# Kernel optimization log

Measured on AMD Instinct MI355X. Metric: run time of the kernel, lower is better.

## Reference

```python
import jax, jax.numpy as jnp
import numpy as np


def setup_inputs() -> dict:
    key = jax.random.key(0)
    ks = jax.random.split(key, 10)
    B, N, K, F, H, C, L = 2, 20000, 32, 128, 128, 40, 3
    return {
        "vertex_feat": jax.random.uniform(ks[0], (B, N, F), dtype=jnp.float32),
        "neighbors_idx": jax.random.randint(ks[1], (B, N, K), 0, N, dtype=jnp.int32),
        "valid_lens": jax.random.randint(ks[2], (B, N), 0, K + 1, dtype=jnp.int32),
        "W_embed": jax.random.normal(ks[3], (F, H), dtype=jnp.float32) * 0.05,
        "gcn_W": jax.random.normal(ks[4], (L, H, H), dtype=jnp.float32) * 0.05,
        "gcn_B": jax.random.normal(ks[5], (L, H, H), dtype=jnp.float32) * 0.05,
        "cls_W1": jax.random.normal(ks[6], (H, H), dtype=jnp.float32) * 0.05,
        "cls_b1": jnp.zeros((H,), dtype=jnp.float32),
        "cls_W2": jax.random.normal(ks[7], (H, C), dtype=jnp.float32) * 0.05,
        "cls_b2": jnp.zeros((C,), dtype=jnp.float32),
    }


def reference(vertex_feat, neighbors_idx, valid_lens, W_embed, gcn_W, gcn_B,
              cls_W1, cls_b1, cls_W2, cls_b2):
    # --- input embedding: Dense(no bias) / row-sum of raw features ---
    row_sum = jnp.sum(vertex_feat, axis=-1, keepdims=True)          # [B,N,1]
    h = jnp.einsum('bnf,fh->bnh', vertex_feat, W_embed) / row_sum   # [B,N,H]

    # valid_lens with zeros replaced by 1, as float divisor
    vl = jnp.where(valid_lens == 0, 1, valid_lens)
    vl = vl.astype(jnp.float32)[..., None]                          # [B,N,1]

    num_layers = gcn_W.shape[0]
    for l in range(num_layers):
        # gather-sum neighbor features (per-graph gather, batch_dims=1)
        neigh = jax.vmap(lambda feat, idx: feat[idx])(h, neighbors_idx)  # [B,N,K,H]
        neigh = jnp.sum(neigh, axis=2) / vl                              # [B,N,H]
        h = jax.nn.relu(jnp.einsum('bnh,hd->bnd', neigh, gcn_W[l])
                        + jnp.einsum('bnh,hd->bnd', h, gcn_B[l]))

    # --- classifier MLP (dropout inactive at inference) ---
    z = jax.nn.relu(jnp.einsum('bnh,hd->bnd', h, cls_W1) + cls_b1)
    logits = jnp.einsum('bnd,dc->bnc', z, cls_W2) + cls_b2
    return jax.nn.softmax(logits, axis=-1)
```

## Files before the change

kernel.cpp:

```cpp
#include <hip/hip_runtime.h>
#include <hip/hip_bf16.h>

typedef __hip_bfloat16 bf16;
typedef __attribute__((ext_vector_type(8))) short short8;
typedef __attribute__((ext_vector_type(4))) float f32x4;

#define NB    20000
#define BATCH 2
#define HDIM  128
#define KNBR  32
#define NCLS  40
#define NLAYER 3
#define BM    64
#define LBM   32
#define LDP   136
#define NTILES 625
#define LTPH   625
#define LGRID  1256

__device__ __forceinline__ short f2bf(float v) {
    return __builtin_bit_cast(short, __float2bfloat16(v));
}
__device__ __forceinline__ float blo(unsigned u) { return __builtin_bit_cast(float, u << 16); }
__device__ __forceinline__ float bhi(unsigned u) { return __builtin_bit_cast(float, u & 0xffff0000u); }

__global__ void pack_weights(const float* __restrict__ Wemb, const float* __restrict__ gW,
                             const float* __restrict__ gB, const float* __restrict__ W1,
                             const float* __restrict__ W2, short* __restrict__ pw) {
    const int idx = blockIdx.x * 256 + threadIdx.x;
    if (idx < 8 * 16384) {
        const int m = idx >> 14, e = idx & 16383;
        const float* src = (m == 0) ? Wemb
                         : (m <= 3) ? gW + (size_t)(m - 1) * 16384
                         : (m <= 6) ? gB + (size_t)(m - 4) * 16384
                         : W1;
        const int k = e >> 7, n = e & 127;
        pw[m * 16384 + (((k >> 3) * 128 + n) << 3) + (k & 7)] = f2bf(src[e]);
    } else {
        const int e = idx - 8 * 16384;
        if (e < 128 * NCLS) {
            const int k = e / NCLS, n = e - k * NCLS;
            pw[8 * 16384 + ((k >> 3) * NCLS + n) * 8 + (k & 7)] = f2bf(W2[e]);
        }
    }
}

__global__ __launch_bounds__(512, 4) void embed_gemm(const float* __restrict__ x,
                                                     const short* __restrict__ pwE,
                                                     bf16* __restrict__ h0) {
    __shared__ short sx[BM * LDP];
    const int t = threadIdx.x;
    const int row0 = blockIdx.x * BM;

    {
        const int r = t >> 3, fs = (t & 7) * 16;
        const float4* p = (const float4*)(x + (size_t)(row0 + r) * HDIM + fs);
        float4 v[4];
#pragma unroll
        for (int i = 0; i < 4; ++i) v[i] = p[i];
        const float* vf = (const float*)v;
        unsigned* dst = (unsigned*)(sx + r * LDP + fs);
#pragma unroll
        for (int i = 0; i < 8; ++i) {
            unsigned lo = (unsigned)(unsigned short)f2bf(vf[2 * i]);
            unsigned hi = (unsigned)(unsigned short)f2bf(vf[2 * i + 1]);
            dst[i] = lo | (hi << 16);
        }
    }
    __syncthreads();

    const int w = t >> 6, l = t & 63;
    const int m16 = l & 15, quad = l >> 4;
    const int col = w * 16 + m16;

    short8 ones;
#pragma unroll
    for (int j = 0; j < 8; ++j) ones[j] = (short)0x3F80;

    short8 wf[4];
#pragma unroll
    for (int q = 0; q < 4; ++q)
        wf[q] = *(const short8*)(pwE + (((q * 4 + quad) * 128 + col) << 3));

    f32x4 acc[4] = {}, rsum[4] = {};
#pragma unroll
    for (int q = 0; q < 4; ++q)
#pragma unroll
        for (int mt = 0; mt < 4; ++mt) {
            short8 a = *(const short8*)(sx + (mt * 16 + m16) * LDP + q * 32 + quad * 8);
            acc[mt]  = __builtin_amdgcn_mfma_f32_16x16x32_bf16(a, wf[q], acc[mt], 0, 0, 0);
            rsum[mt] = __builtin_amdgcn_mfma_f32_16x16x32_bf16(a, ones,  rsum[mt], 0, 0, 0);
        }

#pragma unroll
    for (int mt = 0; mt < 4; ++mt)
#pragma unroll
        for (int r = 0; r < 4; ++r) {
            const int rr = row0 + mt * 16 + quad * 4 + r;
            h0[(size_t)rr * HDIM + col] = __float2bfloat16(acc[mt][r] / rsum[mt][r]);
        }
}

__global__ __launch_bounds__(256, 4) void layer_gemm(const bf16* __restrict__ h_in,
                                                     const int* __restrict__ nidx,
                                                     const int* __restrict__ vlen,
                                                     const short* __restrict__ pwW,
                                                     const short* __restrict__ pwB,
                                                     bf16* __restrict__ h_out) {
    __shared__ int   sidx[LBM * KNBR];
    __shared__ short sng[LBM * LDP];
    __shared__ short sh[LBM * LDP];

    const int slot = blockIdx.x & 7;
    const int half = slot >> 2;
    const int idx  = (blockIdx.x >> 3) * 4 + (slot & 3);
    if (idx >= LTPH) return;
    const int tile = half * LTPH + idx;

    const int t = threadIdx.x;
    const int row0 = tile * LBM;

    ((int4*)sidx)[t] = ((const int4*)(nidx + (size_t)row0 * KNBR))[t];
    {
        const int r = t >> 3, fs = (t & 7) * 16;
        const uint4* p = (const uint4*)(h_in + (size_t)(row0 + r) * HDIM + fs);
        uint4 a = p[0], b = p[1];
        uint4* d = (uint4*)(sh + r * LDP + fs);
        d[0] = a; d[1] = b;
    }
    __syncthreads();

    {
        const int node = t >> 3;
        const int fs8 = (t & 7) * 8;
        const int g = row0 + node;
        const bf16* hb = h_in + (size_t)((g >= NB) ? NB : 0) * HDIM;
        const int* ip = sidx + node * KNBR;
        int vl = vlen[g]; if (vl == 0) vl = 1;
        const float inv = 1.0f / (float)vl;

#pragma unroll
        for (int fh = 0; fh < 2; ++fh) {
            const int fs = fh * 64 + fs8;
            float acc[8];
#pragma unroll
            for (int i = 0; i < 8; ++i) acc[i] = 0.0f;
#pragma unroll 4
            for (int k = 0; k < KNBR; ++k) {
                const uint4 u = *(const uint4*)(hb + (size_t)ip[k] * HDIM + fs);
                acc[0] += blo(u.x); acc[1] += bhi(u.x);
                acc[2] += blo(u.y); acc[3] += bhi(u.y);
                acc[4] += blo(u.z); acc[5] += bhi(u.z);
                acc[6] += blo(u.w); acc[7] += bhi(u.w);
            }
            unsigned* dst = (unsigned*)(sng + node * LDP + fs);
#pragma unroll
            for (int i = 0; i < 4; ++i) {
                unsigned lo = (unsigned)(unsigned short)f2bf(acc[2 * i] * inv);
                unsigned hi = (unsigned)(unsigned short)f2bf(acc[2 * i + 1] * inv);
                dst[i] = lo | (hi << 16);
            }
            __syncthreads();
        }
    }

    const int w = t >> 6, l = t & 63;
    const int m16 = l & 15, quad = l >> 4;
    const int ncol0 = w * 32;

    short8 wfW[2][4], wfB[2][4];
#pragma unroll
    for (int nt = 0; nt < 2; ++nt) {
        const int col = ncol0 + nt * 16 + m16;
#pragma unroll
        for (int q = 0; q < 4; ++q) {
            const int off = ((q * 4 + quad) * 128 + col) << 3;
            wfW[nt][q] = *(const short8*)(pwW + off);
            wfB[nt][q] = *(const short8*)(pwB + off);
        }
    }

    f32x4 acc[2][2] = {};
#pragma unroll
    for (int q = 0; q < 4; ++q)
#pragma unroll
        for (int mt = 0; mt < 2; ++mt) {
            short8 aN = *(const short8*)(sng + (mt * 16 + m16) * LDP + q * 32 + quad * 8);
            short8 aH = *(const short8*)(sh  + (mt * 16 + m16) * LDP + q * 32 + quad * 8);
#pragma unroll
            for (int nt = 0; nt < 2; ++nt) {
                acc[mt][nt] = __builtin_amdgcn_mfma_f32_16x16x32_bf16(aN, wfW[nt][q], acc[mt][nt], 0, 0, 0);
                acc[mt][nt] = __builtin_amdgcn_mfma_f32_16x16x32_bf16(aH, wfB[nt][q], acc[mt][nt], 0, 0, 0);
            }
        }

#pragma unroll
    for (int mt = 0; mt < 2; ++mt)
#pragma unroll
        for (int nt = 0; nt < 2; ++nt)
#pragma unroll
            for (int r = 0; r < 4; ++r) {
                const int rr = row0 + mt * 16 + quad * 4 + r;
                const int cc = ncol0 + nt * 16 + m16;
                h_out[(size_t)rr * HDIM + cc] = __float2bfloat16(fmaxf(acc[mt][nt][r], 0.0f));
            }
}

__global__ __launch_bounds__(512, 4) void cls_gemm(const bf16* __restrict__ h,
                                                   const short* __restrict__ pwW1,
                                                   const float* __restrict__ b1,
                                                   const short* __restrict__ pwW2,
                                                   const float* __restrict__ b2,
                                                   float* __restrict__ out) {
    __shared__ short sh[BM * LDP];
    __shared__ short sz[BM * LDP];
    __shared__ float lg[BM * 48];
    const int t = threadIdx.x;
    const int row0 = blockIdx.x * BM;

    {
        const int r = t >> 3, fs = (t & 7) * 16;
        const uint4* p = (const uint4*)(h + (size_t)(row0 + r) * HDIM + fs);
        uint4 a = p[0], b = p[1];
        uint4* d = (uint4*)(sh + r * LDP + fs);
        d[0] = a; d[1] = b;
    }
    __syncthreads();

    const int w = t >> 6, l = t & 63;
    const int m16 = l & 15, quad = l >> 4;
    const int col = w * 16 + m16;

    {
        short8 wf[4];
#pragma unroll
        for (int q = 0; q < 4; ++q)
            wf[q] = *(const short8*)(pwW1 + (((q * 4 + quad) * 128 + col) << 3));
        f32x4 acc[4] = {};
#pragma unroll
        for (int q = 0; q < 4; ++q)
#pragma unroll
            for (int mt = 0; mt < 4; ++mt) {
                short8 a = *(const short8*)(sh + (mt * 16 + m16) * LDP + q * 32 + quad * 8);
                acc[mt] = __builtin_amdgcn_mfma_f32_16x16x32_bf16(a, wf[q], acc[mt], 0, 0, 0);
            }
        const float bias = b1[col];
#pragma unroll
        for (int mt = 0; mt < 4; ++mt)
#pragma unroll
            for (int r = 0; r < 4; ++r)
                sz[(mt * 16 + quad * 4 + r) * LDP + col] = f2bf(fmaxf(acc[mt][r] + bias, 0.0f));
    }
    __syncthreads();

    if (w < 3) {
        const bool valid = (col < NCLS);
        short8 wf[4];
#pragma unroll
        for (int q = 0; q < 4; ++q) {
            if (valid) wf[q] = *(const short8*)(pwW2 + (((q * 4 + quad) * NCLS + col) << 3));
            else {
#pragma unroll
                for (int j = 0; j < 8; ++j) wf[q][j] = 0;
            }
        }
        f32x4 acc[4] = {};
#pragma unroll
        for (int q = 0; q < 4; ++q)
#pragma unroll
            for (int mt = 0; mt < 4; ++mt) {
                short8 a = *(const short8*)(sz + (mt * 16 + m16) * LDP + q * 32 + quad * 8);
                acc[mt] = __builtin_amdgcn_mfma_f32_16x16x32_bf16(a, wf[q], acc[mt], 0, 0, 0);
            }
        if (valid) {
            const float bias = b2[col];
#pragma unroll
            for (int mt = 0; mt < 4; ++mt)
#pragma unroll
                for (int r = 0; r < 4; ++r)
                    lg[(mt * 16 + quad * 4 + r) * 48 + col] = acc[mt][r] + bias;
        }
    }
    __syncthreads();

    if (t < BM) {
        float* row = lg + t * 48;
        float m = row[0];
        for (int c = 1; c < NCLS; ++c) m = fmaxf(m, row[c]);
        float s = 0.0f;
        for (int c = 0; c < NCLS; ++c) { float e = expf(row[c] - m); row[c] = e; s += e; }
        const float inv = 1.0f / s;
        for (int c = 0; c < NCLS; ++c) row[c] *= inv;
    }
    __syncthreads();

    for (int i = t; i < BM * NCLS; i += 512) {
        const int r = i / NCLS, c = i - r * NCLS;
        out[(size_t)row0 * NCLS + i] = lg[r * 48 + c];
    }
}

extern "C" void kernel_launch(void* const* d_in, const int* in_sizes, int n_in,
                              void* d_out, int out_size, void* d_ws, size_t ws_size,
                              hipStream_t stream) {
    const float* x    = (const float*)d_in[0];
    const int*  nidx  = (const int*)  d_in[1];
    const int*  vlen  = (const int*)  d_in[2];
    const float* Wemb = (const float*)d_in[3];
    const float* gW   = (const float*)d_in[4];
    const float* gB   = (const float*)d_in[5];
    const float* W1   = (const float*)d_in[6];
    const float* b1   = (const float*)d_in[7];
    const float* W2   = (const float*)d_in[8];
    const float* b2   = (const float*)d_in[9];
    float* out = (float*)d_out;

    const int nodes = BATCH * NB;
    bf16* h0 = (bf16*)d_ws;
    bf16* h1 = h0 + (size_t)nodes * HDIM;
    short* pw = (short*)(h1 + (size_t)nodes * HDIM);
    const short* pwE  = pw;
    const short* pwW1 = pw + 7 * 16384;
    const short* pwW2 = pw + 8 * 16384;

    pack_weights<<<(8 * 16384 + 128 * NCLS + 255) / 256, 256, 0, stream>>>(Wemb, gW, gB, W1, W2, pw);
    embed_gemm<<<NTILES, 512, 0, stream>>>(x, pwE, h0);

    for (int lyr = 0; lyr < NLAYER; ++lyr) {
        layer_gemm<<<LGRID, 256, 0, stream>>>(h0, nidx, vlen,
                                              pw + (size_t)(1 + lyr) * 16384,
                                              pw + (size_t)(4 + lyr) * 16384,
                                              h1);
        bf16* tmp = h0; h0 = h1; h1 = tmp;
    }

    cls_gemm<<<NTILES, 512, 0, stream>>>(h0, pwW1, b1, pwW2, b2, out);
}
```

Before: 169.5 us.

## Gather neighbor features from a scaled FP8 copy of node embeddings

Each producer kernel now also writes an FP8 (scaled by 256) copy of the hidden features, and the layer kernel's neighbor gather reads 16 FP8 values per 16-byte load instead of 8 bf16 values. This halves the bytes moved by the random-access gather, which is the dominant memory cost, and removes one loop pass and barrier. It costs an extra byte-wise store per element and gives lower precision in the aggregated neighbor sums, which could matter for accuracy tolerance.

```diff
diff --git a/kernel.cpp b/kernel.cpp
--- a/kernel.cpp
+++ b/kernel.cpp
@@ -4,6 +4,7 @@
 typedef __hip_bfloat16 bf16;
 typedef __attribute__((ext_vector_type(8))) short short8;
 typedef __attribute__((ext_vector_type(4))) float f32x4;
+typedef __attribute__((ext_vector_type(2))) float f32x2;
 
 #define NB    20000
 #define BATCH 2
@@ -17,12 +18,15 @@
 #define NTILES 625
 #define LTPH   625
 #define LGRID  1256
+#define H8SCALE 256.0f
+#define H8INV  (1.0f/256.0f)
 
 __device__ __forceinline__ short f2bf(float v) {
     return __builtin_bit_cast(short, __float2bfloat16(v));
 }
-__device__ __forceinline__ float blo(unsigned u) { return __builtin_bit_cast(float, u << 16); }
-__device__ __forceinline__ float bhi(unsigned u) { return __builtin_bit_cast(float, u & 0xffff0000u); }
+__device__ __forceinline__ unsigned char f2fp8(float v) {
+    return (unsigned char)(__builtin_amdgcn_cvt_pk_fp8_f32(v, 0.0f, 0, false) & 0xff);
+}
 
 __global__ void pack_weights(const float* __restrict__ Wemb, const float* __restrict__ gW,
                              const float* __restrict__ gB, const float* __restrict__ W1,
@@ -47,7 +51,8 @@
 
 __global__ __launch_bounds__(512, 4) void embed_gemm(const float* __restrict__ x,
                                                      const short* __restrict__ pwE,
-                                                     bf16* __restrict__ h0) {
+                                                     bf16* __restrict__ h0,
+                                                     unsigned char* __restrict__ h8) {
     __shared__ short sx[BM * LDP];
     const int t = threadIdx.x;
     const int row0 = blockIdx.x * BM;
@@ -97,16 +102,20 @@
 #pragma unroll
         for (int r = 0; r < 4; ++r) {
             const int rr = row0 + mt * 16 + quad * 4 + r;
-            h0[(size_t)rr * HDIM + col] = __float2bfloat16(acc[mt][r] / rsum[mt][r]);
+            const float v = acc[mt][r] / rsum[mt][r];
+            h0[(size_t)rr * HDIM + col] = __float2bfloat16(v);
+            h8[(size_t)rr * HDIM + col] = f2fp8(v * H8SCALE);
         }
 }
 
 __global__ __launch_bounds__(256, 4) void layer_gemm(const bf16* __restrict__ h_in,
+                                                     const unsigned char* __restrict__ h8_in,
                                                      const int* __restrict__ nidx,
                                                      const int* __restrict__ vlen,
                                                      const short* __restrict__ pwW,
                                                      const short* __restrict__ pwB,
-                                                     bf16* __restrict__ h_out) {
+                                                     bf16* __restrict__ h_out,
+                                                     unsigned char* __restrict__ h8_out) {
     __shared__ int   sidx[LBM * KNBR];
     __shared__ short sng[LBM * LDP];
     __shared__ short sh[LBM * LDP];
@@ -132,37 +141,38 @@
 
     {
         const int node = t >> 3;
-        const int fs8 = (t & 7) * 8;
+        const int fs16 = (t & 7) * 16;
         const int g = row0 + node;
-        const bf16* hb = h_in + (size_t)((g >= NB) ? NB : 0) * HDIM;
+        const unsigned char* hb8 = h8_in + (size_t)((g >= NB) ? NB : 0) * HDIM;
         const int* ip = sidx + node * KNBR;
         int vl = vlen[g]; if (vl == 0) vl = 1;
-        const float inv = 1.0f / (float)vl;
-
-#pragma unroll
-        for (int fh = 0; fh < 2; ++fh) {
-            const int fs = fh * 64 + fs8;
-            float acc[8];
-#pragma unroll
-            for (int i = 0; i < 8; ++i) acc[i] = 0.0f;
+        const float sc = H8INV / (float)vl;
+
+        float acc[16];
+#pragma unroll
+        for (int i = 0; i < 16; ++i) acc[i] = 0.0f;
 #pragma unroll 4
-            for (int k = 0; k < KNBR; ++k) {
-                const uint4 u = *(const uint4*)(hb + (size_t)ip[k] * HDIM + fs);
-                acc[0] += blo(u.x); acc[1] += bhi(u.x);
-                acc[2] += blo(u.y); acc[3] += bhi(u.y);
-                acc[4] += blo(u.z); acc[5] += bhi(u.z);
-                acc[6] += blo(u.w); acc[7] += bhi(u.w);
-            }
-            unsigned* dst = (unsigned*)(sng + node * LDP + fs);
-#pragma unroll
-            for (int i = 0; i < 4; ++i) {
-                unsigned lo = (unsigned)(unsigned short)f2bf(acc[2 * i] * inv);
-                unsigned hi = (unsigned)(unsigned short)f2bf(acc[2 * i + 1] * inv);
-                dst[i] = lo | (hi << 16);
-            }
-            __syncthreads();
-        }
-    }
+        for (int k = 0; k < KNBR; ++k) {
+            const uint4 u = *(const uint4*)(hb8 + (size_t)ip[k] * HDIM + fs16);
+            f32x2 p;
+            p = __builtin_amdgcn_cvt_pk_f32_fp8(u.x, false); acc[0] += p.x;  acc[1] += p.y;
+            p = __builtin_amdgcn_cvt_pk_f32_fp8(u.x, true);  acc[2] += p.x;  acc[3] += p.y;
+            p = __builtin_amdgcn_cvt_pk_f32_fp8(u.y, false); acc[4] += p.x;  acc[5] += p.y;
+            p = __builtin_amdgcn_cvt_pk_f32_fp8(u.y, true);  acc[6] += p.x;  acc[7] += p.y;
+            p = __builtin_amdgcn_cvt_pk_f32_fp8(u.z, false); acc[8] += p.x;  acc[9] += p.y;
+            p = __builtin_amdgcn_cvt_pk_f32_fp8(u.z, true);  acc[10] += p.x; acc[11] += p.y;
+            p = __builtin_amdgcn_cvt_pk_f32_fp8(u.w, false); acc[12] += p.x; acc[13] += p.y;
+            p = __builtin_amdgcn_cvt_pk_f32_fp8(u.w, true);  acc[14] += p.x; acc[15] += p.y;
+        }
+        unsigned* dst = (unsigned*)(sng + node * LDP + fs16);
+#pragma unroll
+        for (int i = 0; i < 8; ++i) {
+            unsigned lo = (unsigned)(unsigned short)f2bf(acc[2 * i] * sc);
+            unsigned hi = (unsigned)(unsigned short)f2bf(acc[2 * i + 1] * sc);
+            dst[i] = lo | (hi << 16);
+        }
+    }
+    __syncthreads();
 
     const int w = t >> 6, l = t & 63;
     const int m16 = l & 15, quad = l >> 4;
@@ -202,7 +212,9 @@
             for (int r = 0; r < 4; ++r) {
                 const int rr = row0 + mt * 16 + quad * 4 + r;
                 const int cc = ncol0 + nt * 16 + m16;
-                h_out[(size_t)rr * HDIM + cc] = __float2bfloat16(fmaxf(acc[mt][nt][r], 0.0f));
+                const float v = fmaxf(acc[mt][nt][r], 0.0f);
+                h_out[(size_t)rr * HDIM + cc] = __float2bfloat16(v);
+                h8_out[(size_t)rr * HDIM + cc] = f2fp8(v * H8SCALE);
             }
 }
 
@@ -318,20 +330,23 @@
     const int nodes = BATCH * NB;
     bf16* h0 = (bf16*)d_ws;
     bf16* h1 = h0 + (size_t)nodes * HDIM;
-    short* pw = (short*)(h1 + (size_t)nodes * HDIM);
+    unsigned char* h8a = (unsigned char*)(h1 + (size_t)nodes * HDIM);
+    unsigned char* h8b = h8a + (size_t)nodes * HDIM;
+    short* pw = (short*)(h8b + (size_t)nodes * HDIM);
     const short* pwE  = pw;
     const short* pwW1 = pw + 7 * 16384;
     const short* pwW2 = pw + 8 * 16384;
 
     pack_weights<<<(8 * 16384 + 128 * NCLS + 255) / 256, 256, 0, stream>>>(Wemb, gW, gB, W1, W2, pw);
-    embed_gemm<<<NTILES, 512, 0, stream>>>(x, pwE, h0);
+    embed_gemm<<<NTILES, 512, 0, stream>>>(x, pwE, h0, h8a);
 
     for (int lyr = 0; lyr < NLAYER; ++lyr) {
-        layer_gemm<<<LGRID, 256, 0, stream>>>(h0, nidx, vlen,
+        layer_gemm<<<LGRID, 256, 0, stream>>>(h0, h8a, nidx, vlen,
                                               pw + (size_t)(1 + lyr) * 16384,
                                               pw + (size_t)(4 + lyr) * 16384,
-                                              h1);
+                                              h1, h8b);
         bf16* tmp = h0; h0 = h1; h1 = tmp;
+        unsigned char* t8 = h8a; h8a = h8b; h8b = t8;
     }
 
     cls_gemm<<<NTILES, 512, 0, stream>>>(h0, pwW1, b1, pwW2, b2, out);
```

New measurement: 173.7 us. 1.02x slower.
